# Kernel optimization log

Measured on AMD Instinct MI355X. Metric: run time of the kernel, lower is better.

The kernel has to match this reference:

```python
import jax, jax.numpy as jnp
import numpy as np

IN_F = 128
OUT_F = 128


def setup_inputs() -> dict:
    key = jax.random.key(0)
    k_x, k_wb, k_bb, k_ww, k_bw = jax.random.split(key, 5)
    s = 1.0 / np.sqrt(IN_F)
    return {
        "x": jax.random.normal(k_x, (4, 2048, IN_F), dtype=jnp.float32),
        "Wb": jax.random.normal(k_wb, (IN_F, OUT_F), dtype=jnp.float32) * s,
        "bb": jax.random.normal(k_bb, (OUT_F,), dtype=jnp.float32) * s,
        "Ww": jax.random.normal(k_ww, (IN_F, IN_F * OUT_F), dtype=jnp.float32) * s,
        "bw": jax.random.normal(k_bw, (IN_F * OUT_F,), dtype=jnp.float32) * s,
    }


def reference(x, Wb, bb, Ww, bw):
    shape = x.shape
    xf = x.reshape(-1, IN_F)                      # [N, in]
    b = xf @ Wb + bb                              # [N, out]
    W = (xf @ Ww + bw).reshape(-1, IN_F, OUT_F)   # [N, in, out] (large)
    y = jnp.einsum('ni,nio->no', xf, W) + b       # batched vec-mat (M=1 bmm)
    return y.reshape(shape[:-1] + (OUT_F,))
```

## Files before the change

kernel.cpp:

```cpp
#include <hip/hip_runtime.h>
#include <stdint.h>
#include <stddef.h>


#define NROWS   8192
#define NKT     516
#define TILE_E  4096
#define XS_STRIDE 136
#define LS_STRIDE 136
#define BM      128
#define NSLICE  8

typedef unsigned short u16;
typedef short short8 __attribute__((ext_vector_type(8)));
typedef unsigned short ushort8 __attribute__((ext_vector_type(8)));
typedef float floatx4 __attribute__((ext_vector_type(4)));

__device__ __align__(16) u16   g_B[(size_t)NKT * TILE_E];
__device__ __align__(16) float g_P[(size_t)NSLICE * NROWS * 128];

__device__ __forceinline__ u16 f2bf_rne(float f) {
    unsigned int u = __float_as_uint(f);
    u += 0x7fffu + ((u >> 16) & 1u);
    return (u16)(u >> 16);
}

__global__ __launch_bounds__(256) void prep_kernel(
    const float* __restrict__ Ww, const float* __restrict__ Wb,
    const float* __restrict__ bw)
{
    __shared__ __align__(16) u16 ls[32 * LS_STRIDE];
    const int kt = blockIdx.x;
    const int t  = threadIdx.x;

    float v[16];
    if (kt < 512) {
        const float* src = Ww + (size_t)(kt >> 2)*16384 + (size_t)(kt & 3)*32*128 + t*16;
#pragma unroll
        for (int c = 0; c < 4; ++c) {
            const floatx4 f4 = *(const floatx4*)(src + c*4);
#pragma unroll
            for (int e = 0; e < 4; ++e) v[c*4 + e] = f4[e];
        }
    } else {
        const size_t base = (size_t)(kt - 512)*32*128 + t*16;
        const float* s1 = Wb + base;
        const float* s2 = bw + base;
#pragma unroll
        for (int c = 0; c < 4; ++c) {
            const floatx4 a = *(const floatx4*)(s1 + c*4);
            const floatx4 b = *(const floatx4*)(s2 + c*4);
#pragma unroll
            for (int e = 0; e < 4; ++e) v[c*4 + e] = a[e] + b[e];
        }
    }
    {
        const int kk = t >> 3;
        const int o0 = (t & 7) * 16;
        ushort8 w0, w1;
#pragma unroll
        for (int e = 0; e < 8; ++e) { w0[e] = f2bf_rne(v[e]); w1[e] = f2bf_rne(v[8+e]); }
        *(ushort8*)&ls[kk*LS_STRIDE + o0]     = w0;
        *(ushort8*)&ls[kk*LS_STRIDE + o0 + 8] = w1;
    }
    __syncthreads();
    {
        const int o   = t >> 1;
        const int kk0 = (t & 1) * 16;
        ushort8 w0, w1;
#pragma unroll
        for (int e = 0; e < 8; ++e) {
            w0[e] = ls[(kk0 + e)*LS_STRIDE + o];
            w1[e] = ls[(kk0 + 8 + e)*LS_STRIDE + o];
        }
        u16* outp = g_B + (size_t)kt*TILE_E + t*16;
        ((ushort8*)outp)[0] = w0; ((ushort8*)outp)[1] = w1;
    }
}

__global__ __launch_bounds__(256)
__attribute__((amdgpu_waves_per_eu(2, 8)))
void gemm_kernel(const float* __restrict__ x)
{
    __shared__ __align__(16) u16 xs[BM * XS_STRIDE];

    const int b     = blockIdx.x;
    const int slice = b >> 7;
    const int rem   = b & 127;
    const int rb    = rem >> 1;
    const int cg    = rem & 1;
    const int row0  = rb * BM;
    const int tid   = threadIdx.x;
    const int lane  = tid & 63;
    const int wave  = tid >> 6;
    const int wm    = wave >> 1;
    const int wc    = wave & 1;
    const int l15   = lane & 15;
    const int q     = lane >> 4;

#pragma unroll
    for (int it = 0; it < 8; ++it) {
        const int c  = it*256 + tid;
        const int r  = c >> 4;
        const int c8 = (c & 15) * 8;
        const float* sp = x + ((size_t)(row0 + r) << 7) + c8;
        const floatx4 f0 = *(const floatx4*)(sp);
        const floatx4 f1 = *(const floatx4*)(sp + 4);
        ushort8 w;
#pragma unroll
        for (int e = 0; e < 4; ++e) { w[e] = f2bf_rne(f0[e]); w[4+e] = f2bf_rne(f1[e]); }
        *(ushort8*)&xs[r*XS_STRIDE + c8] = w;
    }
    __syncthreads();

    short8 af[4][4];
#pragma unroll
    for (int ks = 0; ks < 4; ++ks)
#pragma unroll
        for (int mt = 0; mt < 4; ++mt)
            af[ks][mt] = *(const short8*)&xs[(wm*64 + mt*16 + l15)*XS_STRIDE + ks*32 + q*8];

    const floatx4 fzero = {0.f, 0.f, 0.f, 0.f};
    floatx4 acc[4][2];
#pragma unroll
    for (int i = 0; i < 4; ++i) { acc[i][0] = fzero; acc[i][1] = fzero; }

    const int p0 = slice*16 + (slice ? 1 : 0);
    const int np = slice ? 16 : 17;

    const int colbase = cg*64 + wc*32;
    const size_t loff = (size_t)(colbase + l15)*32 + q*8;
    const int ktN = (p0 + np)*4;

    auto LOADB = [&](int ktl, short8* dst) {
        const u16* tb = g_B + (size_t)ktl*TILE_E + loff;
        dst[0] = *(const short8*)(tb);
        dst[1] = *(const short8*)(tb + 512);
    };

    short8 Abuf[4][2], Bbuf[4][2];

#define DO_PHASE(CUR, NXT, PIDX, KTNXT)                                               \
    {                                                                                  \
        _Pragma("unroll")                                                              \
        for (int s = 0; s < 4; ++s) {                                                  \
            const int kl = (KTNXT) + s;                                                \
            LOADB(kl < ktN ? kl : ktN - 1, NXT[s]);                                    \
        }                                                                              \
        floatx4 aj[4][2];                                                              \
        _Pragma("unroll")                                                              \
        for (int mt = 0; mt < 4; ++mt) {                           \
            aj[mt][0] = __builtin_amdgcn_mfma_f32_16x16x32_bf16(af[0][mt], CUR[0][0], fzero, 0,0,0); \
            aj[mt][1] = __builtin_amdgcn_mfma_f32_16x16x32_bf16(af[0][mt], CUR[0][1], fzero, 0,0,0); \
        }                                                                              \
        _Pragma("unroll")                                                              \
        for (int mt = 0; mt < 4; ++mt) {                                               \
            aj[mt][0] = __builtin_amdgcn_mfma_f32_16x16x32_bf16(af[1][mt], CUR[1][0], aj[mt][0], 0,0,0); \
            aj[mt][1] = __builtin_amdgcn_mfma_f32_16x16x32_bf16(af[1][mt], CUR[1][1], aj[mt][1], 0,0,0); \
        }                                                                              \
        _Pragma("unroll")                                                              \
        for (int mt = 0; mt < 4; ++mt) {                                               \
            aj[mt][0] = __builtin_amdgcn_mfma_f32_16x16x32_bf16(af[2][mt], CUR[2][0], aj[mt][0], 0,0,0); \
            aj[mt][1] = __builtin_amdgcn_mfma_f32_16x16x32_bf16(af[2][mt], CUR[2][1], aj[mt][1], 0,0,0); \
        }                                                                              \
        _Pragma("unroll")                                                              \
        for (int mt = 0; mt < 4; ++mt) {                                               \
            aj[mt][0] = __builtin_amdgcn_mfma_f32_16x16x32_bf16(af[3][mt], CUR[3][0], aj[mt][0], 0,0,0); \
            aj[mt][1] = __builtin_amdgcn_mfma_f32_16x16x32_bf16(af[3][mt], CUR[3][1], aj[mt][1], 0,0,0); \
        }                                                                              \
        _Pragma("unroll")                                                              \
        for (int mt = 0; mt < 4; ++mt) {                                               \
            _Pragma("unroll")                                                          \
            for (int r = 0; r < 4; ++r) {                                              \
                const int rl = wm*64 + mt*16 + q*4 + r;      \
                float xj = 1.0f;                                                       \
                if ((PIDX) < 128)                                                      \
                    xj = __uint_as_float(((unsigned int)xs[rl*XS_STRIDE + (PIDX)]) << 16); \
                acc[mt][0][r] += xj * aj[mt][0][r];                                    \
                acc[mt][1][r] += xj * aj[mt][1][r];                                    \
            }                                                                          \
        }                                                                              \
    }

    int kt = p0*4;
#pragma unroll
    for (int s = 0; s < 4; ++s) LOADB(kt + s, Abuf[s]);

    const int pairs = np >> 1;
    for (int j = 0; j < pairs; ++j) {
        const int p = p0 + 2*j;
        DO_PHASE(Abuf, Bbuf, p,     kt + 4);
        DO_PHASE(Bbuf, Abuf, p + 1, kt + 8);
        kt += 8;
    }
    if (np & 1) {
        const int p = p0 + np - 1;
        DO_PHASE(Abuf, Bbuf, p, kt + 4);
    }
#undef DO_PHASE

    float* op = g_P + (size_t)slice * ((size_t)NROWS * 128);
#pragma unroll
    for (int mt = 0; mt < 4; ++mt)
#pragma unroll
        for (int nt = 0; nt < 2; ++nt) {
            const int col = colbase + nt*16 + l15;
#pragma unroll
            for (int r = 0; r < 4; ++r) {
                const int row = row0 + wm*64 + mt*16 + q*4 + r;
                op[((size_t)row << 7) + col] = acc[mt][nt][r];
            }
        }
}

__global__ __launch_bounds__(256) void finish_kernel(
    const float* __restrict__ bb, float* __restrict__ out)
{
    const int flat = (blockIdx.x*256 + threadIdx.x) * 8;
    floatx4 s0 = {0.f, 0.f, 0.f, 0.f};
    floatx4 s1 = {0.f, 0.f, 0.f, 0.f};
#pragma unroll
    for (int s = 0; s < NSLICE; ++s) {
        const float* p = g_P + (size_t)s * ((size_t)NROWS * 128) + flat;
        const floatx4 a = *(const floatx4*)p;
        const floatx4 c = *(const floatx4*)(p + 4);
#pragma unroll
        for (int e = 0; e < 4; ++e) { s0[e] += a[e]; s1[e] += c[e]; }
    }
    const floatx4 b0 = *(const floatx4*)(bb + (flat & 127));
    const floatx4 b1 = *(const floatx4*)(bb + (flat & 127) + 4);
    floatx4 o0, o1;
#pragma unroll
    for (int e = 0; e < 4; ++e) { o0[e] = s0[e] + b0[e]; o1[e] = s1[e] + b1[e]; }
    *(floatx4*)(out + flat)     = o0;
    *(floatx4*)(out + flat + 4) = o1;
}

extern "C" void kernel_launch(void* const* d_in, const int* in_sizes, int n_in,
                              void* d_out, int out_size, void* d_ws, size_t ws_size,
                              hipStream_t stream) {
    (void)in_sizes; (void)n_in; (void)out_size; (void)d_ws; (void)ws_size;
    const float* x  = (const float*)d_in[0];
    const float* Wb = (const float*)d_in[1];
    const float* bb = (const float*)d_in[2];
    const float* Ww = (const float*)d_in[3];
    const float* bw = (const float*)d_in[4];
    float* out = (float*)d_out;

    prep_kernel  <<<dim3(NKT),            dim3(256), 0, stream>>>(Ww, Wb, bw);
    gemm_kernel  <<<dim3(1024),           dim3(256), 0, stream>>>(x);
    finish_kernel<<<dim3(NROWS*128/2048), dim3(256), 0, stream>>>(bb, out);
}
```

Before: 120.2 us.

## Replace split-K partial buffer and finish kernel with atomic accumulation into output

The prep kernel now also writes the bias bb into the output. The gemm kernel atomically adds its per-slice partial sums straight into the output, which removes the 8-slice partial buffer g_P and the separate reduction kernel. This saves a kernel launch and the write and reread of the partial buffer. In exchange it adds 8-way atomic contention per output element and makes the float summation order nondeterministic. The per-row x scaling in the accumulation loop is also rewritten as vector multiply-adds.

```diff
diff --git a/kernel.cpp b/kernel.cpp
--- a/kernel.cpp
+++ b/kernel.cpp
@@ -16,8 +16,7 @@
 typedef unsigned short ushort8 __attribute__((ext_vector_type(8)));
 typedef float floatx4 __attribute__((ext_vector_type(4)));
 
-__device__ __align__(16) u16   g_B[(size_t)NKT * TILE_E];
-__device__ __align__(16) float g_P[(size_t)NSLICE * NROWS * 128];
+__device__ __align__(16) u16 g_B[(size_t)NKT * TILE_E];
 
 __device__ __forceinline__ u16 f2bf_rne(float f) {
     unsigned int u = __float_as_uint(f);
@@ -27,11 +26,20 @@
 
 __global__ __launch_bounds__(256) void prep_kernel(
     const float* __restrict__ Ww, const float* __restrict__ Wb,
-    const float* __restrict__ bw)
+    const float* __restrict__ bw, const float* __restrict__ bb,
+    float* __restrict__ out)
 {
     __shared__ __align__(16) u16 ls[32 * LS_STRIDE];
     const int kt = blockIdx.x;
     const int t  = threadIdx.x;
+
+    if (kt < 512) {
+        const int flat = (kt*256 + t) * 8;
+        const floatx4 b0 = *(const floatx4*)(bb + (flat & 127));
+        const floatx4 b1 = *(const floatx4*)(bb + (flat & 127) + 4);
+        *(floatx4*)(out + flat)     = b0;
+        *(floatx4*)(out + flat + 4) = b1;
+    }
 
     float v[16];
     if (kt < 512) {
@@ -80,7 +88,7 @@
 
 __global__ __launch_bounds__(256)
 __attribute__((amdgpu_waves_per_eu(2, 8)))
-void gemm_kernel(const float* __restrict__ x)
+void gemm_kernel(const float* __restrict__ x, float* __restrict__ out)
 {
     __shared__ __align__(16) u16 xs[BM * XS_STRIDE];
 
@@ -170,15 +178,16 @@
         }                                                                              \
         _Pragma("unroll")                                                              \
         for (int mt = 0; mt < 4; ++mt) {                                               \
+            floatx4 xjv;                                                               \
             _Pragma("unroll")                                                          \
             for (int r = 0; r < 4; ++r) {                                              \
                 const int rl = wm*64 + mt*16 + q*4 + r;      \
-                float xj = 1.0f;                                                       \
-                if ((PIDX) < 128)                                                      \
-                    xj = __uint_as_float(((unsigned int)xs[rl*XS_STRIDE + (PIDX)]) << 16); \
-                acc[mt][0][r] += xj * aj[mt][0][r];                                    \
-                acc[mt][1][r] += xj * aj[mt][1][r];                                    \
+                xjv[r] = ((PIDX) < 128)                                                \
+                    ? __uint_as_float(((unsigned int)xs[rl*XS_STRIDE + (PIDX)]) << 16) \
+                    : 1.0f;                                                            \
             }                                                                          \
+            acc[mt][0] += xjv * aj[mt][0];                                             \
+            acc[mt][1] += xjv * aj[mt][1];                                             \
         }                                                                              \
     }
 
@@ -199,7 +208,6 @@
     }
 #undef DO_PHASE
 
-    float* op = g_P + (size_t)slice * ((size_t)NROWS * 128);
 #pragma unroll
     for (int mt = 0; mt < 4; ++mt)
 #pragma unroll
@@ -208,32 +216,9 @@
 #pragma unroll
             for (int r = 0; r < 4; ++r) {
                 const int row = row0 + wm*64 + mt*16 + q*4 + r;
-                op[((size_t)row << 7) + col] = acc[mt][nt][r];
+                atomicAdd(&out[((size_t)row << 7) + col], acc[mt][nt][r]);
             }
         }
-}
-
-__global__ __launch_bounds__(256) void finish_kernel(
-    const float* __restrict__ bb, float* __restrict__ out)
-{
-    const int flat = (blockIdx.x*256 + threadIdx.x) * 8;
-    floatx4 s0 = {0.f, 0.f, 0.f, 0.f};
-    floatx4 s1 = {0.f, 0.f, 0.f, 0.f};
-#pragma unroll
-    for (int s = 0; s < NSLICE; ++s) {
-        const float* p = g_P + (size_t)s * ((size_t)NROWS * 128) + flat;
-        const floatx4 a = *(const floatx4*)p;
-        const floatx4 c = *(const floatx4*)(p + 4);
-#pragma unroll
-        for (int e = 0; e < 4; ++e) { s0[e] += a[e]; s1[e] += c[e]; }
-    }
-    const floatx4 b0 = *(const floatx4*)(bb + (flat & 127));
-    const floatx4 b1 = *(const floatx4*)(bb + (flat & 127) + 4);
-    floatx4 o0, o1;
-#pragma unroll
-    for (int e = 0; e < 4; ++e) { o0[e] = s0[e] + b0[e]; o1[e] = s1[e] + b1[e]; }
-    *(floatx4*)(out + flat)     = o0;
-    *(floatx4*)(out + flat + 4) = o1;
 }
 
 extern "C" void kernel_launch(void* const* d_in, const int* in_sizes, int n_in,
@@ -247,7 +232,6 @@
     const float* bw = (const float*)d_in[4];
     float* out = (float*)d_out;
 
-    prep_kernel  <<<dim3(NKT),            dim3(256), 0, stream>>>(Ww, Wb, bw);
-    gemm_kernel  <<<dim3(1024),           dim3(256), 0, stream>>>(x);
-    finish_kernel<<<dim3(NROWS*128/2048), dim3(256), 0, stream>>>(bb, out);
-}
+    prep_kernel<<<dim3(NKT),  dim3(256), 0, stream>>>(Ww, Wb, bw, bb, out);
+    gemm_kernel<<<dim3(1024), dim3(256), 0, stream>>>(x, out);
+}
```

Result: slower. 127.2 us (+5.8%).
